# Kernel optimization log

Hardware: AMD Instinct MI355X
Metric: run time of the kernel (lower is better)

Reference implementation:

```python
import jax, jax.numpy as jnp
import numpy as np

N, D_IN, D_OUT, E, TOPK = 2048, 2048, 2048, 8, 2


def setup_inputs() -> dict:
    key = jax.random.key(0)
    k1, k2, k3, k4 = jax.random.split(key, 4)
    inputs = jax.random.normal(k1, (N, D_IN), dtype=jnp.float32)
    weight = jax.random.normal(k2, (E, D_OUT, D_IN), dtype=jnp.float32) * (1.0 / np.sqrt(D_IN))
    gates = jax.random.uniform(k3, (N, TOPK), dtype=jnp.float32)
    gates = gates / jnp.sum(gates, axis=-1, keepdims=True)
    # random routing: expert id for each of the N*TOPK (token, slot) pairs
    expert_of = jax.random.randint(k4, (N * TOPK,), 0, E, dtype=jnp.int32)
    order = jnp.argsort(expert_of)  # positions sorted by expert id
    sorted_expert_idxs = expert_of[order].astype(jnp.int32)
    sorted_scattered_idxs = order.astype(jnp.int32)
    counts = jnp.bincount(expert_of, length=E)
    expert_offsets = jnp.cumsum(counts).astype(jnp.int32)
    padded_block_idxs = jnp.zeros((1,), dtype=jnp.int32)  # kernel blocking artifact, no math effect
    return {
        "inputs": inputs,
        "weight": weight,
        "k": TOPK,
        "sorted_expert_idxs": sorted_expert_idxs,
        "sorted_scattered_idxs": sorted_scattered_idxs,
        "padded_block_idxs": padded_block_idxs,
        "expert_offsets": expert_offsets,
        "gates": gates,
    }


def reference(inputs, weight, k, sorted_expert_idxs, sorted_scattered_idxs,
              padded_block_idxs, expert_offsets, gates):
    # inputs: [N, d_in]; weight: [E, d_out, d_in] (module permutes to [E, d_in, d_out])
    n_tok, d_in = inputs.shape
    n_e, d_out, _ = weight.shape
    nk = sorted_expert_idxs.shape[0]
    # invert the sort: expert id per flat (token, slot) position
    expert_of = jnp.zeros((nk,), dtype=sorted_expert_idxs.dtype).at[sorted_scattered_idxs].set(sorted_expert_idxs)
    x_flat = inputs[jnp.arange(nk) // k]  # [N*k, d_in] (fan-out of k per token)
    # grouped GEMM: y_flat[j] = x_flat[j] @ weight[expert_of[j]].T
    y_flat = jnp.zeros((nk, d_out), dtype=inputs.dtype)
    for e in range(n_e):  # loop over fixed small expert count (structural)
        mask = (expert_of == e)[:, None]
        y_flat = y_flat + jnp.where(mask, x_flat, 0.0) @ weight[e].T
    # gating combine: bmm(gates[:, None, :], y.view(N, k, d_out))
    out = jnp.einsum('nk,nkd->nd', gates, y_flat.reshape(n_tok, k, d_out))
    return out
```

## Files before the change

### kernel.cpp

```cpp
#include <hip/hip_runtime.h>
#include <hip/hip_bf16.h>

#define DIN   2048
#define DOUT  2048
#define NTOK  2048
#define NE    8
#define TOPK  2
#define NK    (NTOK*TOPK)
#define BM    128
#define BN    128
#define BK    64
#define NKT   (DIN/BK)
#define MAXMT (NK/BM + NE)
#define NTN   (DOUT/BN)
#define NBLK  (MAXMT*NTN)

#define WEL (NE*DOUT*DIN)
#define XEL (NTOK*DIN)

typedef unsigned short u16;
typedef __attribute__((ext_vector_type(8))) short bf16x8;
typedef __attribute__((ext_vector_type(4))) float f32x4;

__device__ __forceinline__ unsigned pack2rn(float a, float b) {
    union { float f; unsigned u; } x, y; x.f = a; y.f = b;
    return __builtin_amdgcn_perm(y.u + 0x8000u, x.u + 0x8000u, 0x07060302u);
}

__device__ __forceinline__ void gl_lds16(const void* g, void* l) {
    __builtin_amdgcn_global_load_lds(
        (const __attribute__((address_space(1))) void*)g,
        (__attribute__((address_space(3)))       void*)l, 16, 0, 0);
}

__global__ __launch_bounds__(256) void cvt_x(
    const float* __restrict__ x, u16* __restrict__ xbf)
{
    const size_t nch = (size_t)XEL / 8;
    for (size_t c = (size_t)blockIdx.x * blockDim.x + threadIdx.x; c < nch;
         c += (size_t)gridDim.x * blockDim.x) {
        size_t off = c * 8;
        float4 f0 = *(const float4*)(x + off);
        float4 f1 = *(const float4*)(x + off + 4);
        uint4 pk;
        pk.x = pack2rn(f0.x, f0.y); pk.y = pack2rn(f0.z, f0.w);
        pk.z = pack2rn(f1.x, f1.y); pk.w = pack2rn(f1.z, f1.w);
        *(uint4*)(xbf + off) = pk;
    }
}

__global__ __launch_bounds__(512, 4) void moe_gemm_wf(
    const u16*   __restrict__ xb,
    const float* __restrict__ wf,
    const int*   __restrict__ sorted_scattered_idxs,
    const int*   __restrict__ expert_offsets,
    const float* __restrict__ gates,
    float*       __restrict__ out)
{
    __shared__ u16 As[2][BM * BK];
    __shared__ u16 Bs[2][BN * BK];
    __shared__ int   s_tok[BM];
    __shared__ float s_gate[BM];

    const int bid = blockIdx.x;
    const int swz = (bid & 7) * (NBLK / 8) + (bid >> 3);
    const int n0  = (swz & (NTN - 1)) * BN;
    const int mt  = swz >> 4;

    int e = -1, m0 = 0, cnt = 0;
    {
        int acc0 = 0, prev = 0;
        for (int i = 0; i < NE; ++i) {
            int end = expert_offsets[i];
            int c = end - prev;
            int t = (c + BM - 1) / BM;
            if (mt < acc0 + t) {
                e = i; m0 = prev + (mt - acc0) * BM;
                cnt = end - m0; if (cnt > BM) cnt = BM;
                break;
            }
            acc0 += t; prev = end;
        }
    }
    if (e < 0) return;

    const int tid = threadIdx.x;
    if (tid < BM) {
        int idx = (tid < cnt) ? (m0 + tid) : m0;
        int p = sorted_scattered_idxs[idx];
        s_tok[tid]  = p;
        s_gate[tid] = gates[p];
    }
    __syncthreads();

    const int wid = tid >> 6, lane = tid & 63;

    const int ch   = tid & 7;
    const int row0 = tid >> 3;
    const int cg   = ch ^ (row0 & 7);
    const u16* aS[2];
    #pragma unroll
    for (int s = 0; s < 2; ++s)
        aS[s] = xb + (size_t)(s_tok[row0 + s * 64] >> 1) * DIN + cg * 8;
    const int dst0 = wid * 512;
    const int dst1 = wid * 512 + 4096;

    const float* wbE = wf + (size_t)e * DOUT * DIN;
    const float* bF[2];
    #pragma unroll
    for (int s = 0; s < 2; ++s)
        bF[s] = wbE + (size_t)(n0 + row0 + s * 64) * DIN + ch * 8;
    const int bwr0 = row0 * BK + cg * 8;
    const int bwr1 = (row0 + 64) * BK + cg * 8;

    const int wr = wid >> 2, wc = wid & 3;
    const int lr = lane & 15, g = lane >> 4;
    const int xk0 = ((0 + g) ^ (lr & 7)) * 8;
    const int xk1 = ((4 + g) ^ (lr & 7)) * 8;
    int aoff[4], boff[2];
    #pragma unroll
    for (int mi = 0; mi < 4; ++mi) aoff[mi] = (wr * 64 + mi * 16 + lr) * BK;
    #pragma unroll
    for (int n = 0; n < 2; ++n)    boff[n]  = (wc * 32 + n * 16 + lr) * BK;

    f32x4 acc[4][2];
    #pragma unroll
    for (int mi = 0; mi < 4; ++mi)
        #pragma unroll
        for (int n = 0; n < 2; ++n) acc[mi][n] = (f32x4)0.0f;

    float4 pb[4];

#define STGA(buf, t)                                                          \
    {                                                                         \
        const int ko = (t) * BK;                                              \
        gl_lds16(aS[0] + ko, &As[buf][dst0]);                                 \
        gl_lds16(aS[1] + ko, &As[buf][dst1]);                                 \
    }

#define BGLB(t)                                                               \
    {                                                                         \
        const int ko = (t) * BK;                                              \
        pb[0] = *(const float4*)(bF[0] + ko);                                 \
        pb[1] = *(const float4*)(bF[0] + ko + 4);                             \
        pb[2] = *(const float4*)(bF[1] + ko);                                 \
        pb[3] = *(const float4*)(bF[1] + ko + 4);                             \
    }

#define BPACK(buf)                                                            \
    {                                                                         \
        uint4 w0, w1;                                                         \
        w0.x = pack2rn(pb[0].x, pb[0].y); w0.y = pack2rn(pb[0].z, pb[0].w);   \
        w0.z = pack2rn(pb[1].x, pb[1].y); w0.w = pack2rn(pb[1].z, pb[1].w);   \
        w1.x = pack2rn(pb[2].x, pb[2].y); w1.y = pack2rn(pb[2].z, pb[2].w);   \
        w1.z = pack2rn(pb[3].x, pb[3].y); w1.w = pack2rn(pb[3].z, pb[3].w);   \
        *(uint4*)(&Bs[buf][bwr0]) = w0;                                       \
        *(uint4*)(&Bs[buf][bwr1]) = w1;                                       \
    }

#define BODY(t)                                                               \
    {                                                                         \
        const int b = (t) & 1;                                                \
        bf16x8 af[4][2], bf[2][2];                                            \
        _Pragma("unroll")                                                     \
        for (int mi = 0; mi < 4; ++mi) {                                      \
            af[mi][0] = *(const bf16x8*)(&As[b][aoff[mi] + xk0]);             \
            af[mi][1] = *(const bf16x8*)(&As[b][aoff[mi] + xk1]);             \
        }                                                                     \
        _Pragma("unroll")                                                     \
        for (int n = 0; n < 2; ++n) {                                         \
            bf[n][0] = *(const bf16x8*)(&Bs[b][boff[n] + xk0]);               \
            bf[n][1] = *(const bf16x8*)(&Bs[b][boff[n] + xk1]);               \
        }                                                                     \
        asm volatile("s_waitcnt lgkmcnt(0)" ::: "memory");                    \
        __builtin_amdgcn_sched_barrier(0);                                    \
        __builtin_amdgcn_s_setprio(1);                                        \
        _Pragma("unroll")                                                     \
        for (int mi = 0; mi < 4; ++mi)                                        \
            _Pragma("unroll")                                                 \
            for (int n = 0; n < 2; ++n) {                                     \
                acc[mi][n] = __builtin_amdgcn_mfma_f32_16x16x32_bf16(         \
                    af[mi][0], bf[n][0], acc[mi][n], 0, 0, 0);                \
                acc[mi][n] = __builtin_amdgcn_mfma_f32_16x16x32_bf16(         \
                    af[mi][1], bf[n][1], acc[mi][n], 0, 0, 0);                \
            }                                                                 \
        __builtin_amdgcn_s_setprio(0);                                        \
        __builtin_amdgcn_s_barrier();                                         \
    }

    BGLB(0);
    STGA(0, 0);
    asm volatile("s_waitcnt vmcnt(0)" ::: "memory");
    __builtin_amdgcn_sched_barrier(0);
    BPACK(0);
    STGA(1, 1);
    BGLB(1);

    for (int t = 0; t < NKT; ++t) {
        asm volatile("s_waitcnt lgkmcnt(0)" ::: "memory");
        __builtin_amdgcn_s_barrier();
        BODY(t);
        asm volatile("s_waitcnt vmcnt(0)" ::: "memory");
        __builtin_amdgcn_sched_barrier(0);
        if (t + 1 < NKT) BPACK((t + 1) & 1);
        if (t + 2 < NKT) { STGA(t & 1, t + 2); BGLB(t + 2); }
    }

#undef STGA
#undef BGLB
#undef BPACK
#undef BODY

    #pragma unroll
    for (int mi = 0; mi < 4; ++mi) {
        #pragma unroll
        for (int r = 0; r < 4; ++r) {
            int lrow = wr * 64 + mi * 16 + g * 4 + r;
            if (lrow < cnt) {
                int   p  = s_tok[lrow];
                float gf = s_gate[lrow];
                float* orow = out + (size_t)(p >> 1) * DOUT + n0 + wc * 32;
                #pragma unroll
                for (int n = 0; n < 2; ++n)
                    atomicAdd(orow + n * 16 + lr, gf * acc[mi][n][r]);
            }
        }
    }
}

#define FBM 128
#define FBK 64
__global__ __launch_bounds__(256, 3) void moe_gemm_fused(
    const float* __restrict__ inputs, const float* __restrict__ weight,
    const int* __restrict__ sorted_scattered_idxs, const int* __restrict__ expert_offsets,
    const float* __restrict__ gates, float* __restrict__ out)
{
    __shared__ u16 As[FBM * FBK];
    __shared__ u16 Bs[FBM * FBK];
    __shared__ int   s_tok[FBM];
    __shared__ float s_gate[FBM];

    const int mt = blockIdx.y;
    const int n0 = blockIdx.x * FBM;
    int e = -1, m0 = 0, cnt = 0;
    {
        int acc = 0, prev = 0;
        for (int i = 0; i < NE; ++i) {
            int end = expert_offsets[i];
            int c = end - prev;
            int t = (c + FBM - 1) / FBM;
            if (mt < acc + t) {
                e = i; m0 = prev + (mt - acc) * FBM;
                cnt = end - m0; if (cnt > FBM) cnt = FBM;
                break;
            }
            acc += t; prev = end;
        }
    }
    if (e < 0) return;

    const int tid = threadIdx.x;
    if (tid < FBM) {
        int idx = (tid < cnt) ? (m0 + tid) : m0;
        int p = sorted_scattered_idxs[idx];
        s_tok[tid]  = p;
        s_gate[tid] = gates[p];
    }
    __syncthreads();

    const int ch  = tid & 7;
    const int r0  = tid >> 3;
    const int sch = ch ^ (r0 & 7);
    const float* wbase = weight + (size_t)e * DOUT * DIN;
    const float* ap[4]; const float* bp[4];
    #pragma unroll
    for (int i = 0; i < 4; ++i) {
        int r = r0 + 32 * i;
        ap[i] = inputs + (size_t)(s_tok[r] >> 1) * DIN + ch * 8;
        bp[i] = wbase + (size_t)(n0 + r) * DIN + ch * 8;
    }
    u16* aw = &As[r0 * FBK + sch * 8];
    u16* bw = &Bs[r0 * FBK + sch * 8];

    const int wid = tid >> 6, lane = tid & 63;
    const int wm = (wid >> 1) * 64, wn = (wid & 1) * 64;
    const int g  = lane >> 4, lr = lane & 15;

    f32x4 acc[4][4];
    #pragma unroll
    for (int i = 0; i < 4; ++i)
        #pragma unroll
        for (int j = 0; j < 4; ++j) acc[i][j] = (f32x4)0.0f;

    float4 pa[4][2], pb[4][2];
    #pragma unroll
    for (int i = 0; i < 4; ++i) {
        pa[i][0] = *(const float4*)(ap[i] + 0); pa[i][1] = *(const float4*)(ap[i] + 4);
        pb[i][0] = *(const float4*)(bp[i] + 0); pb[i][1] = *(const float4*)(bp[i] + 4);
    }
    for (int kt = 0; kt < DIN / FBK; ++kt) {
        __syncthreads();
        #pragma unroll
        for (int i = 0; i < 4; ++i) {
            uint4 va, vb;
            va.x = pack2rn(pa[i][0].x, pa[i][0].y); va.y = pack2rn(pa[i][0].z, pa[i][0].w);
            va.z = pack2rn(pa[i][1].x, pa[i][1].y); va.w = pack2rn(pa[i][1].z, pa[i][1].w);
            *(uint4*)(aw + i * 32 * FBK) = va;
            vb.x = pack2rn(pb[i][0].x, pb[i][0].y); vb.y = pack2rn(pb[i][0].z, pb[i][0].w);
            vb.z = pack2rn(pb[i][1].x, pb[i][1].y); vb.w = pack2rn(pb[i][1].z, pb[i][1].w);
            *(uint4*)(bw + i * 32 * FBK) = vb;
        }
        __syncthreads();
        if (kt + 1 < DIN / FBK) {
            const int kof = (kt + 1) * FBK;
            #pragma unroll
            for (int i = 0; i < 4; ++i) {
                pa[i][0] = *(const float4*)(ap[i] + kof); pa[i][1] = *(const float4*)(ap[i] + kof + 4);
                pb[i][0] = *(const float4*)(bp[i] + kof); pb[i][1] = *(const float4*)(bp[i] + kof + 4);
            }
        }
        #pragma unroll
        for (int ks = 0; ks < 2; ++ks) {
            bf16x8 a[4], b[4];
            #pragma unroll
            for (int i = 0; i < 4; ++i) {
                int ra = wm + i * 16 + lr; int ca = (ks * 4 + g) ^ (ra & 7);
                a[i] = *(const bf16x8*)(&As[ra * FBK + ca * 8]);
                int rb = wn + i * 16 + lr; int cb = (ks * 4 + g) ^ (rb & 7);
                b[i] = *(const bf16x8*)(&Bs[rb * FBK + cb * 8]);
            }
            #pragma unroll
            for (int i = 0; i < 4; ++i)
                #pragma unroll
                for (int j = 0; j < 4; ++j)
                    acc[i][j] = __builtin_amdgcn_mfma_f32_16x16x32_bf16(a[i], b[j], acc[i][j], 0, 0, 0);
        }
    }
    #pragma unroll
    for (int i = 0; i < 4; ++i) {
        #pragma unroll
        for (int j2 = 0; j2 < 4; ++j2) {
            int lrow = wm + i * 16 + g * 4 + j2;
            if (lrow < cnt) {
                int   p  = s_tok[lrow];
                float gf = s_gate[lrow];
                float* orow = out + (size_t)(p >> 1) * DOUT + n0 + wn;
                #pragma unroll
                for (int nf = 0; nf < 4; ++nf)
                    atomicAdd(orow + nf * 16 + lr, gf * acc[i][nf][j2]);
            }
        }
    }
}

extern "C" void kernel_launch(void* const* d_in, const int* in_sizes, int n_in,
                              void* d_out, int out_size, void* d_ws, size_t ws_size,
                              hipStream_t stream) {
    const float* inputs  = (const float*)d_in[0];
    const float* weight  = (const float*)d_in[1];
    const int*   ssi     = (const int*)d_in[4];
    const int*   eoff    = (const int*)d_in[6];
    const float* gates   = (const float*)d_in[7];
    float* out = (float*)d_out;

    hipMemsetAsync(out, 0, (size_t)out_size * sizeof(float), stream);

    const size_t need = (size_t)XEL * sizeof(u16);
    if (ws_size >= need) {
        u16* xbf = (u16*)d_ws;
        cvt_x<<<1024, 256, 0, stream>>>(inputs, xbf);
        moe_gemm_wf<<<NBLK, 512, 0, stream>>>(xbf, weight, ssi, eoff, gates, out);
    } else {
        dim3 grid(DOUT / FBM, NK / FBM + NE);
        moe_gemm_fused<<<grid, 256, 0, stream>>>(inputs, weight, ssi, eoff, gates, out);
    }
}
```

Baseline: 113.7 us.

## Double M tile to 256 and halve K tile in MoE grouped GEMM

```diff
diff --git a/kernel.cpp b/kernel.cpp
--- a/kernel.cpp
+++ b/kernel.cpp
@@ -7,9 +7,9 @@
 #define NE    8
 #define TOPK  2
 #define NK    (NTOK*TOPK)
-#define BM    128
+#define BM    256
 #define BN    128
-#define BK    64
+#define BK    32
 #define NKT   (DIN/BK)
 #define MAXMT (NK/BM + NE)
 #define NTN   (DOUT/BN)
@@ -49,7 +49,7 @@
     }
 }
 
-__global__ __launch_bounds__(512, 4) void moe_gemm_wf(
+__global__ __launch_bounds__(512, 4) void moe_gemm_wf2(
     const u16*   __restrict__ xb,
     const float* __restrict__ wf,
     const int*   __restrict__ sorted_scattered_idxs,
@@ -95,95 +95,84 @@
 
     const int wid = tid >> 6, lane = tid & 63;
 
-    const int ch   = tid & 7;
-    const int row0 = tid >> 3;
-    const int cg   = ch ^ (row0 & 7);
-    const u16* aS[2];
-    #pragma unroll
-    for (int s = 0; s < 2; ++s)
-        aS[s] = xb + (size_t)(s_tok[row0 + s * 64] >> 1) * DIN + cg * 8;
-    const int dst0 = wid * 512;
-    const int dst1 = wid * 512 + 4096;
-
-    const float* wbE = wf + (size_t)e * DOUT * DIN;
-    const float* bF[2];
-    #pragma unroll
-    for (int s = 0; s < 2; ++s)
-        bF[s] = wbE + (size_t)(n0 + row0 + s * 64) * DIN + ch * 8;
-    const int bwr0 = row0 * BK + cg * 8;
-    const int bwr1 = (row0 + 64) * BK + cg * 8;
+    const int arow0 = wid * 16 + (lane >> 2);
+    const int cga   = (lane & 3) ^ ((lane >> 3) & 3);
+    const u16* aS0 = xb + (size_t)(s_tok[arow0] >> 1) * DIN + cga * 8;
+    const u16* aS1 = xb + (size_t)(s_tok[arow0 + 128] >> 1) * DIN + cga * 8;
+    const int adst0 = (wid * 16) * BK;
+    const int adst1 = (128 + wid * 16) * BK;
+
+    const int brow = tid >> 2;
+    const int bch  = tid & 3;
+    const int bcg  = bch ^ ((brow >> 1) & 3);
+    const float* bF = wf + (size_t)e * DOUT * DIN + (size_t)(n0 + brow) * DIN + bch * 8;
+    const int bwr = brow * BK + bcg * 8;
 
     const int wr = wid >> 2, wc = wid & 3;
     const int lr = lane & 15, g = lane >> 4;
-    const int xk0 = ((0 + g) ^ (lr & 7)) * 8;
-    const int xk1 = ((4 + g) ^ (lr & 7)) * 8;
-    int aoff[4], boff[2];
-    #pragma unroll
-    for (int mi = 0; mi < 4; ++mi) aoff[mi] = (wr * 64 + mi * 16 + lr) * BK;
-    #pragma unroll
-    for (int n = 0; n < 2; ++n)    boff[n]  = (wc * 32 + n * 16 + lr) * BK;
-
-    f32x4 acc[4][2];
-    #pragma unroll
-    for (int mi = 0; mi < 4; ++mi)
+    const int xch = (g ^ ((lr >> 1) & 3)) * 8;
+    int aoff[8], boff[2];
+    #pragma unroll
+    for (int mi = 0; mi < 8; ++mi) aoff[mi] = (wr * 128 + mi * 16 + lr) * BK + xch;
+    #pragma unroll
+    for (int n = 0; n < 2; ++n)    boff[n]  = (wc * 32 + n * 16 + lr) * BK + xch;
+
+    f32x4 acc[8][2];
+    #pragma unroll
+    for (int mi = 0; mi < 8; ++mi)
         #pragma unroll
         for (int n = 0; n < 2; ++n) acc[mi][n] = (f32x4)0.0f;
 
-    float4 pb[4];
+    float4 pb0, pb1;
 
 #define STGA(buf, t)                                                          \
     {                                                                         \
         const int ko = (t) * BK;                                              \
-        gl_lds16(aS[0] + ko, &As[buf][dst0]);                                 \
-        gl_lds16(aS[1] + ko, &As[buf][dst1]);                                 \
+        gl_lds16(aS0 + ko, &As[buf][adst0]);                                  \
+        gl_lds16(aS1 + ko, &As[buf][adst1]);                                  \
     }
 
 #define BGLB(t)                                                               \
     {                                                                         \
         const int ko = (t) * BK;                                              \
-        pb[0] = *(const float4*)(bF[0] + ko);                                 \
-        pb[1] = *(const float4*)(bF[0] + ko + 4);                             \
-        pb[2] = *(const float4*)(bF[1] + ko);                                 \
-        pb[3] = *(const float4*)(bF[1] + ko + 4);                             \
+        pb0 = *(const float4*)(bF + ko);                                      \
+        pb1 = *(const float4*)(bF + ko + 4);                                  \
     }
 
 #define BPACK(buf)                                                            \
     {                                                                         \
-        uint4 w0, w1;                                                         \
-        w0.x = pack2rn(pb[0].x, pb[0].y); w0.y = pack2rn(pb[0].z, pb[0].w);   \
-        w0.z = pack2rn(pb[1].x, pb[1].y); w0.w = pack2rn(pb[1].z, pb[1].w);   \
-        w1.x = pack2rn(pb[2].x, pb[2].y); w1.y = pack2rn(pb[2].z, pb[2].w);   \
-        w1.z = pack2rn(pb[3].x, pb[3].y); w1.w = pack2rn(pb[3].z, pb[3].w);   \
-        *(uint4*)(&Bs[buf][bwr0]) = w0;                                       \
-        *(uint4*)(&Bs[buf][bwr1]) = w1;                                       \
-    }
-
-#define BODY(t)                                                               \
+        uint4 w;                                                              \
+        w.x = pack2rn(pb0.x, pb0.y); w.y = pack2rn(pb0.z, pb0.w);             \
+        w.z = pack2rn(pb1.x, pb1.y); w.w = pack2rn(pb1.z, pb1.w);             \
+        *(uint4*)(&Bs[buf][bwr]) = w;                                         \
+    }
+
+#define BODY(b)                                                               \
     {                                                                         \
-        const int b = (t) & 1;                                                \
-        bf16x8 af[4][2], bf[2][2];                                            \
+        bf16x8 bfv[2], af[4], ag[4];                                          \
+        bfv[0] = *(const bf16x8*)(&Bs[b][boff[0]]);                           \
+        bfv[1] = *(const bf16x8*)(&Bs[b][boff[1]]);                           \
+        _Pragma("unroll")                                                     \
+        for (int mi = 0; mi < 4; ++mi)                                        \
+            af[mi] = *(const bf16x8*)(&As[b][aoff[mi]]);                      \
+        __builtin_amdgcn_s_setprio(1);                                        \
         _Pragma("unroll")                                                     \
         for (int mi = 0; mi < 4; ++mi) {                                      \
-            af[mi][0] = *(const bf16x8*)(&As[b][aoff[mi] + xk0]);             \
-            af[mi][1] = *(const bf16x8*)(&As[b][aoff[mi] + xk1]);             \
+            acc[mi][0] = __builtin_amdgcn_mfma_f32_16x16x32_bf16(             \
+                af[mi], bfv[0], acc[mi][0], 0, 0, 0);                         \
+            acc[mi][1] = __builtin_amdgcn_mfma_f32_16x16x32_bf16(             \
+                af[mi], bfv[1], acc[mi][1], 0, 0, 0);                         \
         }                                                                     \
         _Pragma("unroll")                                                     \
-        for (int n = 0; n < 2; ++n) {                                         \
-            bf[n][0] = *(const bf16x8*)(&Bs[b][boff[n] + xk0]);               \
-            bf[n][1] = *(const bf16x8*)(&Bs[b][boff[n] + xk1]);               \
+        for (int mi = 0; mi < 4; ++mi)                                        \
+            ag[mi] = *(const bf16x8*)(&As[b][aoff[mi + 4]]);                  \
+        _Pragma("unroll")                                                     \
+        for (int mi = 0; mi < 4; ++mi) {                                      \
+            acc[mi+4][0] = __builtin_amdgcn_mfma_f32_16x16x32_bf16(           \
+                ag[mi], bfv[0], acc[mi+4][0], 0, 0, 0);                       \
+            acc[mi+4][1] = __builtin_amdgcn_mfma_f32_16x16x32_bf16(           \
+                ag[mi], bfv[1], acc[mi+4][1], 0, 0, 0);                       \
         }                                                                     \
-        asm volatile("s_waitcnt lgkmcnt(0)" ::: "memory");                    \
-        __builtin_amdgcn_sched_barrier(0);                                    \
-        __builtin_amdgcn_s_setprio(1);                                        \
-        _Pragma("unroll")                                                     \
-        for (int mi = 0; mi < 4; ++mi)                                        \
-            _Pragma("unroll")                                                 \
-            for (int n = 0; n < 2; ++n) {                                     \
-                acc[mi][n] = __builtin_amdgcn_mfma_f32_16x16x32_bf16(         \
-                    af[mi][0], bf[n][0], acc[mi][n], 0, 0, 0);                \
-                acc[mi][n] = __builtin_amdgcn_mfma_f32_16x16x32_bf16(         \
-                    af[mi][1], bf[n][1], acc[mi][n], 0, 0, 0);                \
-            }                                                                 \
         __builtin_amdgcn_s_setprio(0);                                        \
         __builtin_amdgcn_s_barrier();                                         \
     }
@@ -196,10 +185,11 @@
     STGA(1, 1);
     BGLB(1);
 
+    #pragma unroll 2
     for (int t = 0; t < NKT; ++t) {
         asm volatile("s_waitcnt lgkmcnt(0)" ::: "memory");
         __builtin_amdgcn_s_barrier();
-        BODY(t);
+        BODY(t & 1);
         asm volatile("s_waitcnt vmcnt(0)" ::: "memory");
         __builtin_amdgcn_sched_barrier(0);
         if (t + 1 < NKT) BPACK((t + 1) & 1);
@@ -212,10 +202,10 @@
 #undef BODY
 
     #pragma unroll
-    for (int mi = 0; mi < 4; ++mi) {
+    for (int mi = 0; mi < 8; ++mi) {
         #pragma unroll
         for (int r = 0; r < 4; ++r) {
-            int lrow = wr * 64 + mi * 16 + g * 4 + r;
+            int lrow = wr * 128 + mi * 16 + g * 4 + r;
             if (lrow < cnt) {
                 int   p  = s_tok[lrow];
                 float gf = s_gate[lrow];
@@ -369,7 +359,7 @@
     if (ws_size >= need) {
         u16* xbf = (u16*)d_ws;
         cvt_x<<<1024, 256, 0, stream>>>(inputs, xbf);
-        moe_gemm_wf<<<NBLK, 512, 0, stream>>>(xbf, weight, ssi, eoff, gates, out);
+        moe_gemm_wf2<<<NBLK, 512, 0, stream>>>(xbf, weight, ssi, eoff, gates, out);
     } else {
         dim3 grid(DOUT / FBM, NK / FBM + NE);
         moe_gemm_fused<<<grid, 256, 0, stream>>>(inputs, weight, ssi, eoff, gates, out);
```

New measurement: 109.0 us. -4.2%, faster.
